# Performance work log

Hardware: AMD Instinct MI355X
Metric: run time of the kernel (lower is better)

Reference implementation:

```python
import jax, jax.numpy as jnp
import numpy as np

BETA = 0.9
THRESHOLD = 1.0
SLOPE = 25.0


def _heaviside(x):
    return (x > 0).astype(x.dtype)


def setup_inputs() -> dict:
    key = jax.random.key(0)
    k = jax.random.split(key, 5)
    B, T, I, H, C = 256, 500, 256, 512, 8
    x = jax.random.normal(k[0], (B, T, I), dtype=jnp.float32)
    W1 = jax.random.normal(k[1], (H, I), dtype=jnp.float32) * (1.0 / np.sqrt(I))
    b1 = jax.random.normal(k[2], (H,), dtype=jnp.float32) * 0.01
    W2 = jax.random.normal(k[3], (C, H), dtype=jnp.float32) * (1.0 / np.sqrt(H))
    b2 = jax.random.normal(k[4], (C,), dtype=jnp.float32) * 0.01
    return {"x": x, "W1": W1, "b1": b1, "W2": W2, "b2": b2}


def reference(x, W1, b1, W2, b2):
    # x: (B, T, I)
    B, T, I = x.shape
    # Time-invariant fc1 batched outside the recurrence: (B, T, H)
    cur1 = jnp.einsum('bti,hi->bth', x, W1) + b1
    cur1_t = jnp.swapaxes(cur1, 0, 1)  # (T, B, H)

    def step(mem, cur):
        # snntorch Leaky (reset_mechanism='subtract'):
        # reset computed from previous mem crossing threshold
        reset = _heaviside(mem - THRESHOLD)
        mem_new = BETA * mem + cur - reset * THRESHOLD
        spk = _heaviside(mem_new - THRESHOLD)
        return mem_new, spk

    mem0 = jnp.zeros((B, W1.shape[0]), dtype=x.dtype)
    _, spks = jax.lax.scan(step, mem0, cur1_t)  # spks: (T, B, H)

    # out_sum = sum_t (spk_t @ W2^T + b2) = (sum_t spk_t) @ W2^T + T*b2
    spk_sum = spks.sum(axis=0)  # (B, H)
    out_sum = spk_sum @ W2.T + jnp.asarray(T, x.dtype) * b2  # (B, C)
    return out_sum
```

## Files before the change

### kernel.cpp

```cpp
#include <hip/hip_runtime.h>


#define B_   256
#define T_   500
#define I_   256
#define H_   512
#define C_   8

#define TC   64
#define BK   32
#define NKS  (I_ / BK)
#define NCH  ((T_ + TC - 1) / TC)
#define DSTR 68

#define WTH_OFF 0
#define WTL_OFF 16384
#define XTH_OFF 32768
#define XTL_OFF 36864

typedef __attribute__((ext_vector_type(8))) _Float16 half8;
typedef __attribute__((ext_vector_type(4))) float f32x4;

union H8 { _Float16 h[8]; float4 v; };

__global__ void init_out_kernel(const float* __restrict__ b2,
                                float* __restrict__ out) {
  int idx = blockIdx.x * 256 + threadIdx.x;
  if (idx < B_ * C_) out[idx] = (float)T_ * b2[idx & (C_ - 1)];
}

__global__ void split_w1_kernel(const float* __restrict__ W1,
                                char* __restrict__ ws) {
  int idx = blockIdx.x * 256 + threadIdx.x;
  if (idx >= H_ * I_) return;
  const int h = idx >> 8, i = idx & 255;
  const float w = W1[h * I_ + i];
  const _Float16 hi = (_Float16)w;
  const _Float16 lo = (_Float16)((w - (float)hi) * 2048.0f);
  const int kstep = i >> 5, kk = i & 31, c = kk >> 3, e = kk & 7;
  const int half = h >> 8, hl = h & 255;
  const int slot = ((hl << 2) + c) ^ (hl & 7);
  const size_t off =
      ((size_t)((kstep << 1) + half) << 14) + ((size_t)slot << 4) + (e << 1);
  *(_Float16*)(ws + off) = hi;
  *(_Float16*)(ws + 262144 + off) = lo;
}

__global__ __launch_bounds__(256, 2) void snn_mfma_kernel(
    const float* __restrict__ x, const char* __restrict__ ws,
    const float* __restrict__ b1, const float* __restrict__ W2,
    float* __restrict__ out) {
  __shared__ __align__(16) char smem[40960];

  const int tid  = threadIdx.x;
  const int b    = blockIdx.x;
  const int half = blockIdx.y;

  const int l  = tid & 63;
  const int wv = tid >> 6;
  const int cc = l >> 4;
  const int rr = l & 15;
  const int sw = rr & 7;

  int offA[4], offB[4];
  #pragma unroll
  for (int i = 0; i < 4; ++i)
    offA[i] = (((i << 6) + (rr << 2) + cc) ^ sw) << 4;
  #pragma unroll
  for (int j = 0; j < 4; ++j)
    offB[j] = (((wv << 8) + (j << 6) + (rr << 2) + cc) ^ sw) << 4;

  const int xc = tid & 3, xt = tid >> 2;
  const int xslot = (((xt << 2) + xc) ^ (xt & 7)) << 4;

  const float* xb = x + (size_t)b * (T_ * I_);
  const float biash = b1[(half << 8) + (wv << 6) + l];

  float mreg = 0.f, cnt = 0.f;

  #pragma unroll 1
  for (int ch = 0; ch < NCH; ++ch) {
    const int t0 = ch * TC;

    f32x4 acch[4][4], accl[4][4];
    #pragma unroll
    for (int i = 0; i < 4; ++i)
      #pragma unroll
      for (int j = 0; j < 4; ++j) {
        acch[i][j] = (f32x4){0.f, 0.f, 0.f, 0.f};
        accl[i][j] = (f32x4){0.f, 0.f, 0.f, 0.f};
      }

    #pragma unroll 1
    for (int ks = 0; ks < NKS; ++ks) {
      __syncthreads();
      {
        const char* gh = ws + (((size_t)((ks << 1) + half)) << 14);
        const char* gl = gh + 262144;
        #pragma unroll
        for (int qq = 0; qq < 4; ++qq) {
          const int o = (tid << 4) + (qq << 12);
          *(float4*)(smem + WTH_OFF + o) = *(const float4*)(gh + o);
          *(float4*)(smem + WTL_OFF + o) = *(const float4*)(gl + o);
        }
      }
      {
        H8 h8, l8;
        const int tg = t0 + xt;
        if (tg < T_) {
          const float* xr = xb + (size_t)tg * I_ + (ks << 5) + (xc << 3);
          const float4 a  = *(const float4*)xr;
          const float4 b4 = *(const float4*)(xr + 4);
          const float av[8] = {a.x, a.y, a.z, a.w, b4.x, b4.y, b4.z, b4.w};
          #pragma unroll
          for (int e = 0; e < 8; ++e) {
            const _Float16 hh = (_Float16)av[e];
            h8.h[e] = hh;
            l8.h[e] = (_Float16)((av[e] - (float)hh) * 2048.0f);
          }
        } else {
          #pragma unroll
          for (int e = 0; e < 8; ++e) { h8.h[e] = (_Float16)0.f; l8.h[e] = (_Float16)0.f; }
        }
        *(float4*)(smem + XTH_OFF + xslot) = h8.v;
        *(float4*)(smem + XTL_OFF + xslot) = l8.v;
      }
      __syncthreads();
      half8 ah[4], al[4], bh[4], bl[4];
      #pragma unroll
      for (int i = 0; i < 4; ++i) {
        ah[i] = *(const half8*)(smem + XTH_OFF + offA[i]);
        al[i] = *(const half8*)(smem + XTL_OFF + offA[i]);
      }
      #pragma unroll
      for (int j = 0; j < 4; ++j) {
        bh[j] = *(const half8*)(smem + WTH_OFF + offB[j]);
        bl[j] = *(const half8*)(smem + WTL_OFF + offB[j]);
      }
      #pragma unroll
      for (int i = 0; i < 4; ++i)
        #pragma unroll
        for (int j = 0; j < 4; ++j)
          acch[i][j] = __builtin_amdgcn_mfma_f32_16x16x32_f16(
              ah[i], bh[j], acch[i][j], 0, 0, 0);
      #pragma unroll
      for (int i = 0; i < 4; ++i)
        #pragma unroll
        for (int j = 0; j < 4; ++j) {
          accl[i][j] = __builtin_amdgcn_mfma_f32_16x16x32_f16(
              ah[i], bl[j], accl[i][j], 0, 0, 0);
          accl[i][j] = __builtin_amdgcn_mfma_f32_16x16x32_f16(
              al[i], bh[j], accl[i][j], 0, 0, 0);
        }
    }

    __syncthreads();

    float* dmp = (float*)smem + wv * (32 * DSTR);
    #pragma unroll
    for (int ht = 0; ht < 2; ++ht) {
      #pragma unroll
      for (int i2 = 0; i2 < 2; ++i2) {
        const int i = (ht << 1) + i2;
        #pragma unroll
        for (int j = 0; j < 4; ++j)
          #pragma unroll
          for (int r = 0; r < 4; ++r) {
            const int tl = (i2 << 4) + ((l >> 4) << 2) + r;
            dmp[tl * DSTR + (j << 4) + rr] =
                acch[i][j][r] + 4.8828125e-4f * accl[i][j][r];
          }
      }
      const int base = t0 + (ht << 5);
      int nt = T_ - base; nt = nt < 32 ? nt : 32;
      #pragma unroll 1
      for (int jj = 0; jj < nt; ++jj) {
        const float cur = dmp[jj * DSTR + l] + biash;
        const float rst = (mreg > 1.0f) ? 1.0f : 0.0f;
        mreg = fmaf(0.9f, mreg, cur) - rst;
        if (mreg > 1.0f) cnt += 1.0f;
      }
    }
  }

  const int hglob = (half << 8) + (wv << 6) + l;
  #pragma unroll
  for (int c = 0; c < C_; ++c) {
    float p = cnt * W2[c * H_ + hglob];
    #pragma unroll
    for (int m = 32; m >= 1; m >>= 1) p += __shfl_xor(p, m, 64);
    if (l == 0) atomicAdd(&out[b * C_ + c], p);
  }
}

extern "C" void kernel_launch(void* const* d_in, const int* in_sizes, int n_in,
                              void* d_out, int out_size, void* d_ws,
                              size_t ws_size, hipStream_t stream) {
  (void)in_sizes; (void)n_in; (void)ws_size; (void)out_size;
  const float* x  = (const float*)d_in[0];
  const float* W1 = (const float*)d_in[1];
  const float* b1 = (const float*)d_in[2];
  const float* W2 = (const float*)d_in[3];
  const float* b2 = (const float*)d_in[4];
  float* out = (float*)d_out;
  char* ws = (char*)d_ws;

  init_out_kernel<<<dim3((B_ * C_ + 255) / 256), dim3(256), 0, stream>>>(b2, out);
  split_w1_kernel<<<dim3((H_ * I_ + 255) / 256), dim3(256), 0, stream>>>(W1, ws);
  snn_mfma_kernel<<<dim3(B_, 2), dim3(256), 0, stream>>>(x, ws, b1, W2, out);
}
```

Before: 310.5 us.

## Pipeline x staging with double-buffered LDS and direct global-to-LDS weight DMA

Restructures the fc1 GEMM loop into one flat pipeline over chunk and k-step. Each round prefetches the next x tile into registers and double-buffers it in LDS, loads W1 hi/lo tiles straight into LDS with global_load_lds, and doubles the time chunk to 128. The hi/lo split now uses a single accumulator with a pre-scaling by 16 instead of separate hi and lo accumulators. The spike scan reads from a swizzled float4 dump. The aim is to hide global-load latency and cut accumulator and conversion overhead, at the cost of more registers (32 accumulators plus 16 A fragments) and 64KB of LDS, which may limit occupancy to 2 blocks.

After: 261.2 us. -15.9%, faster.

```diff
diff --git a/kernel.cpp b/kernel.cpp
--- a/kernel.cpp
+++ b/kernel.cpp
@@ -7,21 +7,28 @@
 #define H_   512
 #define C_   8
 
-#define TC   64
+#define TC   128
 #define BK   32
-#define NKS  (I_ / BK)
-#define NCH  ((T_ + TC - 1) / TC)
-#define DSTR 68
-
-#define WTH_OFF 0
-#define WTL_OFF 16384
-#define XTH_OFF 32768
-#define XTL_OFF 36864
+#define NKS  8
+#define NCH  4
+#define NR   (NCH * NKS)
+
+#define WBUF  0
+#define XBUF0 32768
+#define XBUF1 49152
 
 typedef __attribute__((ext_vector_type(8))) _Float16 half8;
+typedef __attribute__((ext_vector_type(2))) __fp16 f16x2;
 typedef __attribute__((ext_vector_type(4))) float f32x4;
 
-union H8 { _Float16 h[8]; float4 v; };
+typedef __attribute__((address_space(1))) const unsigned int as1_uint;
+typedef __attribute__((address_space(3))) unsigned int as3_uint;
+
+__device__ __forceinline__ void lds_dma16(const void* g, void* l) {
+  __builtin_amdgcn_global_load_lds((as1_uint*)g, (as3_uint*)l, 16, 0, 0);
+}
+
+#define MFMA16(A, B, Cc) __builtin_amdgcn_mfma_f32_16x16x32_f16(A, B, Cc, 0, 0, 0)
 
 __global__ void init_out_kernel(const float* __restrict__ b2,
                                 float* __restrict__ out) {
@@ -31,159 +38,187 @@
 
 __global__ void split_w1_kernel(const float* __restrict__ W1,
                                 char* __restrict__ ws) {
-  int idx = blockIdx.x * 256 + threadIdx.x;
-  if (idx >= H_ * I_) return;
-  const int h = idx >> 8, i = idx & 255;
-  const float w = W1[h * I_ + i];
-  const _Float16 hi = (_Float16)w;
-  const _Float16 lo = (_Float16)((w - (float)hi) * 2048.0f);
-  const int kstep = i >> 5, kk = i & 31, c = kk >> 3, e = kk & 7;
-  const int half = h >> 8, hl = h & 255;
-  const int slot = ((hl << 2) + c) ^ (hl & 7);
-  const size_t off =
-      ((size_t)((kstep << 1) + half) << 14) + ((size_t)slot << 4) + (e << 1);
-  *(_Float16*)(ws + off) = hi;
-  *(_Float16*)(ws + 262144 + off) = lo;
-}
-
-__global__ __launch_bounds__(256, 2) void snn_mfma_kernel(
+  const int n = blockIdx.x * 256 + threadIdx.x;
+  if (n >= H_ * NKS * 4) return;
+  const int h = n >> 5, ks = (n >> 2) & 7, c = n & 3;
+  const float* src = W1 + h * I_ + ks * BK + c * 8;
+  union { half8 v; _Float16 e[8]; } hi, lo;
+  #pragma unroll
+  for (int e = 0; e < 8; ++e) {
+    const float w = 16.0f * src[e];
+    const _Float16 wh = (_Float16)w;
+    hi.e[e] = wh;
+    lo.e[e] = (_Float16)(w - (float)wh);
+  }
+  const int slot = (((h & 255) << 2) + c) ^ (h & 7);
+  char* dst = ws + (size_t)((ks << 1) + (h >> 8)) * 32768 + ((size_t)slot << 4);
+  *(half8*)dst = hi.v;
+  *(half8*)(dst + 16384) = lo.v;
+}
+
+__device__ __forceinline__ void load_x16(const float* xb, int t, int ib,
+                                         float* a) {
+  if (t < T_) {
+    const float* xr = xb + (size_t)t * I_ + ib;
+    #pragma unroll
+    for (int q = 0; q < 4; ++q) {
+      const float4 v = *(const float4*)(xr + 4 * q);
+      a[4 * q + 0] = v.x; a[4 * q + 1] = v.y;
+      a[4 * q + 2] = v.z; a[4 * q + 3] = v.w;
+    }
+  } else {
+    #pragma unroll
+    for (int e = 0; e < 16; ++e) a[e] = 0.f;
+  }
+}
+
+__device__ __forceinline__ void cvt_store_x(char* dstbase, int xs0, int xs1,
+                                            const float* a) {
+  union { half8 v; f16x2 p[4]; } h0, h1, l0, l1;
+  #pragma unroll
+  for (int k = 0; k < 4; ++k) {
+    const f16x2 ha = __builtin_amdgcn_cvt_pkrtz(a[2 * k], a[2 * k + 1]);
+    h0.p[k] = ha;
+    l0.p[k] = __builtin_amdgcn_cvt_pkrtz(a[2 * k] - (float)ha[0],
+                                         a[2 * k + 1] - (float)ha[1]);
+    const f16x2 hb = __builtin_amdgcn_cvt_pkrtz(a[8 + 2 * k], a[9 + 2 * k]);
+    h1.p[k] = hb;
+    l1.p[k] = __builtin_amdgcn_cvt_pkrtz(a[8 + 2 * k] - (float)hb[0],
+                                         a[9 + 2 * k] - (float)hb[1]);
+  }
+  *(half8*)(dstbase + xs0) = h0.v;
+  *(half8*)(dstbase + xs1) = h1.v;
+  *(half8*)(dstbase + 8192 + xs0) = l0.v;
+  *(half8*)(dstbase + 8192 + xs1) = l1.v;
+}
+
+__global__ __launch_bounds__(256, 2) void snn_mfma2(
     const float* __restrict__ x, const char* __restrict__ ws,
     const float* __restrict__ b1, const float* __restrict__ W2,
     float* __restrict__ out) {
-  __shared__ __align__(16) char smem[40960];
-
-  const int tid  = threadIdx.x;
-  const int b    = blockIdx.x;
-  const int half = blockIdx.y;
-
-  const int l  = tid & 63;
-  const int wv = tid >> 6;
-  const int cc = l >> 4;
-  const int rr = l & 15;
-  const int sw = rr & 7;
-
-  int offA[4], offB[4];
-  #pragma unroll
-  for (int i = 0; i < 4; ++i)
-    offA[i] = (((i << 6) + (rr << 2) + cc) ^ sw) << 4;
-  #pragma unroll
-  for (int j = 0; j < 4; ++j)
-    offB[j] = (((wv << 8) + (j << 6) + (rr << 2) + cc) ^ sw) << 4;
-
-  const int xc = tid & 3, xt = tid >> 2;
-  const int xslot = (((xt << 2) + xc) ^ (xt & 7)) << 4;
+  __shared__ __align__(16) char smem[65536];
+
+  const int tid = threadIdx.x;
+  const int b = blockIdx.x, half = blockIdx.y;
+  const int l = tid & 63, wv = tid >> 6;
+  const int rr = l & 15, cc = l >> 4;
 
   const float* xb = x + (size_t)b * (T_ * I_);
-  const float biash = b1[(half << 8) + (wv << 6) + l];
-
+
+  const int fsw = (((rr << 2) + cc) ^ (rr & 7)) << 4;
+
+  const int tl = tid >> 1, ih = tid & 1;
+  const int xs0 = ((((tl << 2) + ih * 2 + 0) ^ (tl & 7)) << 4);
+  const int xs1 = ((((tl << 2) + ih * 2 + 1) ^ (tl & 7)) << 4);
+
+  const float bias16 = 16.0f * b1[half * 256 + wv * 64 + l];
   float mreg = 0.f, cnt = 0.f;
 
+  f32x4 acc[8][4];
+  #pragma unroll
+  for (int i = 0; i < 8; ++i)
+    #pragma unroll
+    for (int j = 0; j < 4; ++j) acc[i][j] = (f32x4){0.f, 0.f, 0.f, 0.f};
+
+  {
+    const char* wg = ws + (size_t)half * 32768;
+    #pragma unroll
+    for (int q = 0; q < 8; ++q)
+      lds_dma16(wg + (wv * 8 + q) * 1024 + l * 16,
+                smem + WBUF + (wv * 8 + q) * 1024);
+    float a16[16];
+    load_x16(xb, tl, ih * 16, a16);
+    cvt_store_x(smem + XBUF0, xs0, xs1, a16);
+    __syncthreads();
+  }
+
   #pragma unroll 1
-  for (int ch = 0; ch < NCH; ++ch) {
-    const int t0 = ch * TC;
-
-    f32x4 acch[4][4], accl[4][4];
-    #pragma unroll
-    for (int i = 0; i < 4; ++i)
+  for (int r = 0; r < NR; ++r) {
+    const int ks = r & 7, chunk = r >> 3;
+    const int xcur = XBUF0 + (r & 1) * 16384;
+    const int xnxt = XBUF0 + ((r + 1) & 1) * 16384;
+    const bool do_stage = (r + 1 < NR);
+
+    float a16[16];
+    if (do_stage) {
+      const int t1 = ((r + 1) >> 3) * TC + tl;
+      load_x16(xb, t1, ((r + 1) & 7) * BK + ih * 16, a16);
+    }
+
+    half8 ah[8], al[8], bh[4], bl[4];
+    #pragma unroll
+    for (int i = 0; i < 8; ++i) {
+      ah[i] = *(const half8*)(smem + xcur + i * 1024 + fsw);
+      al[i] = *(const half8*)(smem + xcur + 8192 + i * 1024 + fsw);
+    }
+    #pragma unroll
+    for (int j = 0; j < 4; ++j) {
+      bh[j] = *(const half8*)(smem + WBUF + wv * 4096 + j * 1024 + fsw);
+      bl[j] = *(const half8*)(smem + WBUF + 16384 + wv * 4096 + j * 1024 + fsw);
+    }
+    #pragma unroll
+    for (int i = 0; i < 8; ++i)
       #pragma unroll
       for (int j = 0; j < 4; ++j) {
-        acch[i][j] = (f32x4){0.f, 0.f, 0.f, 0.f};
-        accl[i][j] = (f32x4){0.f, 0.f, 0.f, 0.f};
+        acc[i][j] = MFMA16(ah[i], bh[j], acc[i][j]);
+        acc[i][j] = MFMA16(al[i], bh[j], acc[i][j]);
+        acc[i][j] = MFMA16(ah[i], bl[j], acc[i][j]);
       }
 
-    #pragma unroll 1
-    for (int ks = 0; ks < NKS; ++ks) {
-      __syncthreads();
-      {
-        const char* gh = ws + (((size_t)((ks << 1) + half)) << 14);
-        const char* gl = gh + 262144;
+    if (ks == 7) {
+      asm volatile("" ::: "memory");
+      const int t0 = chunk * TC;
+      #pragma unroll
+      for (int p = 0; p < 4; ++p) {
         #pragma unroll
-        for (int qq = 0; qq < 4; ++qq) {
-          const int o = (tid << 4) + (qq << 12);
-          *(float4*)(smem + WTH_OFF + o) = *(const float4*)(gh + o);
-          *(float4*)(smem + WTL_OFF + o) = *(const float4*)(gl + o);
+        for (int i2 = 0; i2 < 2; ++i2) {
+          #pragma unroll
+          for (int j = 0; j < 4; ++j) {
+            const int rl = j * 16 + rr;
+            const int g = i2 * 4 + cc;
+            const int ad = (rl >> 5) * 16384 + wv * 4096 + (rl & 31) * 128 +
+                           ((g ^ (rl & 7)) << 4);
+            *(f32x4*)(smem + ad) = acc[2 * p + i2][j];
+          }
+        }
+        const int nt = T_ - (t0 + 32 * p) < 32 ? T_ - (t0 + 32 * p) : 32;
+        const int rb = (l >> 5) * 16384 + wv * 4096 + (l & 31) * 128;
+        #pragma unroll
+        for (int g = 0; g < 8; ++g) {
+          if (4 * g < nt) {
+            const float4 v =
+                *(const float4*)(smem + rb + ((g ^ (l & 7)) << 4));
+            const float cv[4] = {v.x, v.y, v.z, v.w};
+            #pragma unroll
+            for (int e = 0; e < 4; ++e) {
+              const float curv = cv[e] + bias16;
+              const float rst = (mreg > 16.0f) ? 16.0f : 0.f;
+              mreg = fmaf(0.9f, mreg, curv) - rst;
+              if (mreg > 16.0f) cnt += 1.f;
+            }
+          }
         }
       }
-      {
-        H8 h8, l8;
-        const int tg = t0 + xt;
-        if (tg < T_) {
-          const float* xr = xb + (size_t)tg * I_ + (ks << 5) + (xc << 3);
-          const float4 a  = *(const float4*)xr;
-          const float4 b4 = *(const float4*)(xr + 4);
-          const float av[8] = {a.x, a.y, a.z, a.w, b4.x, b4.y, b4.z, b4.w};
-          #pragma unroll
-          for (int e = 0; e < 8; ++e) {
-            const _Float16 hh = (_Float16)av[e];
-            h8.h[e] = hh;
-            l8.h[e] = (_Float16)((av[e] - (float)hh) * 2048.0f);
-          }
-        } else {
-          #pragma unroll
-          for (int e = 0; e < 8; ++e) { h8.h[e] = (_Float16)0.f; l8.h[e] = (_Float16)0.f; }
-        }
-        *(float4*)(smem + XTH_OFF + xslot) = h8.v;
-        *(float4*)(smem + XTL_OFF + xslot) = l8.v;
-      }
-      __syncthreads();
-      half8 ah[4], al[4], bh[4], bl[4];
-      #pragma unroll
-      for (int i = 0; i < 4; ++i) {
-        ah[i] = *(const half8*)(smem + XTH_OFF + offA[i]);
-        al[i] = *(const half8*)(smem + XTL_OFF + offA[i]);
-      }
-      #pragma unroll
-      for (int j = 0; j < 4; ++j) {
-        bh[j] = *(const half8*)(smem + WTH_OFF + offB[j]);
-        bl[j] = *(const half8*)(smem + WTL_OFF + offB[j]);
-      }
-      #pragma unroll
-      for (int i = 0; i < 4; ++i)
+      #pragma unroll
+      for (int i = 0; i < 8; ++i)
         #pragma unroll
-        for (int j = 0; j < 4; ++j)
-          acch[i][j] = __builtin_amdgcn_mfma_f32_16x16x32_f16(
-              ah[i], bh[j], acch[i][j], 0, 0, 0);
-      #pragma unroll
-      for (int i = 0; i < 4; ++i)
-        #pragma unroll
-        for (int j = 0; j < 4; ++j) {
-          accl[i][j] = __builtin_amdgcn_mfma_f32_16x16x32_f16(
-              ah[i], bl[j], accl[i][j], 0, 0, 0);
-          accl[i][j] = __builtin_amdgcn_mfma_f32_16x16x32_f16(
-              al[i], bh[j], accl[i][j], 0, 0, 0);
-        }
+        for (int j = 0; j < 4; ++j) acc[i][j] = (f32x4){0.f, 0.f, 0.f, 0.f};
     }
 
     __syncthreads();
 
-    float* dmp = (float*)smem + wv * (32 * DSTR);
-    #pragma unroll
-    for (int ht = 0; ht < 2; ++ht) {
-      #pragma unroll
-      for (int i2 = 0; i2 < 2; ++i2) {
-        const int i = (ht << 1) + i2;
-        #pragma unroll
-        for (int j = 0; j < 4; ++j)
-          #pragma unroll
-          for (int r = 0; r < 4; ++r) {
-            const int tl = (i2 << 4) + ((l >> 4) << 2) + r;
-            dmp[tl * DSTR + (j << 4) + rr] =
-                acch[i][j][r] + 4.8828125e-4f * accl[i][j][r];
-          }
-      }
-      const int base = t0 + (ht << 5);
-      int nt = T_ - base; nt = nt < 32 ? nt : 32;
-      #pragma unroll 1
-      for (int jj = 0; jj < nt; ++jj) {
-        const float cur = dmp[jj * DSTR + l] + biash;
-        const float rst = (mreg > 1.0f) ? 1.0f : 0.0f;
-        mreg = fmaf(0.9f, mreg, cur) - rst;
-        if (mreg > 1.0f) cnt += 1.0f;
-      }
-    }
-  }
-
-  const int hglob = (half << 8) + (wv << 6) + l;
+    if (do_stage) {
+      const char* wg = ws + (size_t)((((r + 1) & 7) << 1) + half) * 32768;
+      #pragma unroll
+      for (int q = 0; q < 8; ++q)
+        lds_dma16(wg + (wv * 8 + q) * 1024 + l * 16,
+                  smem + WBUF + (wv * 8 + q) * 1024);
+      cvt_store_x(smem + xnxt, xs0, xs1, a16);
+    }
+    __syncthreads();
+  }
+
+  const int hglob = half * 256 + wv * 64 + l;
   #pragma unroll
   for (int c = 0; c < C_; ++c) {
     float p = cnt * W2[c * H_ + hglob];
@@ -206,6 +241,6 @@
   char* ws = (char*)d_ws;
 
   init_out_kernel<<<dim3((B_ * C_ + 255) / 256), dim3(256), 0, stream>>>(b2, out);
-  split_w1_kernel<<<dim3((H_ * I_ + 255) / 256), dim3(256), 0, stream>>>(W1, ws);
-  snn_mfma_kernel<<<dim3(B_, 2), dim3(256), 0, stream>>>(x, ws, b1, W2, out);
-}
+  split_w1_kernel<<<dim3(H_ * NKS * 4 / 256), dim3(256), 0, stream>>>(W1, ws);
+  snn_mfma2<<<dim3(B_, 2), dim3(256), 0, stream>>>(x, ws, b1, W2, out);
+}
```
